# Performance work log

Hardware: AMD Instinct MI355X
Metric: run time of the kernel (lower is better)

Reference implementation:

```python
import jax, jax.numpy as jnp
import numpy as np

B, S, H = 512, 14, 128  # batch, encoder seq_len (hardcoded 14 in source), hidden
IN = 1                  # input_size must be 1 (see decoder permute trick)


def lstm_scan(seq, h0, c0, Wih, Whh, b):
    """seq: [T, B, in]. Returns (all_h [T,B,H], h_T, c_T). torch gate order i,f,g,o."""
    def step(carry, x_t):
        h, c = carry
        g = x_t @ Wih + h @ Whh + b              # [B, 4H]
        i, f, gg, o = jnp.split(g, 4, axis=-1)
        c = jax.nn.sigmoid(f) * c + jax.nn.sigmoid(i) * jnp.tanh(gg)
        h = jax.nn.sigmoid(o) * jnp.tanh(c)
        return (h, c), h
    (h, c), hs = jax.lax.scan(step, (h0, c0), seq)
    return hs, h, c


def setup_inputs() -> dict:
    key = jax.random.key(0)
    ks = jax.random.split(key, 12)
    s = 1.0 / np.sqrt(H)
    return {
        "inputs": jax.random.normal(ks[0], (B, S, IN), dtype=jnp.float32),
        "target_len": 8,
        "Wih_e": jax.random.normal(ks[1], (IN, 4 * H), dtype=jnp.float32) * s,
        "Whh_e": jax.random.normal(ks[2], (H, 4 * H), dtype=jnp.float32) * s,
        "b_e":   jax.random.normal(ks[3], (4 * H,), dtype=jnp.float32) * s,
        "Wih_d": jax.random.normal(ks[4], (IN, 4 * H), dtype=jnp.float32) * s,
        "Whh_d": jax.random.normal(ks[5], (H, 4 * H), dtype=jnp.float32) * s,
        "b_d":   jax.random.normal(ks[6], (4 * H,), dtype=jnp.float32) * s,
        "We": jax.random.normal(ks[7], (H, H), dtype=jnp.float32) * s,
        "Wd": jax.random.normal(ks[8], (H, H), dtype=jnp.float32) * s,
        "Wv": jax.random.normal(ks[9], (H, 1), dtype=jnp.float32) * s,
        "Wf": jax.random.normal(ks[10], (H, IN), dtype=jnp.float32) * s,
        "bf": jax.random.normal(ks[11], (IN,), dtype=jnp.float32) * s,
    }


def reference(inputs, target_len, Wih_e, Whh_e, b_e, Wih_d, Whh_d, b_d, We, Wd, Wv, Wf, bf):
    bs = inputs.shape[0]
    h0 = jnp.zeros((bs, H), inputs.dtype)
    c0 = jnp.zeros((bs, H), inputs.dtype)

    # Encoder: LSTM over the S=14 timesteps.
    hs, h_enc, c_enc = lstm_scan(inputs.transpose(1, 0, 2), h0, c0, Wih_e, Whh_e, b_e)
    enc_out = hs.transpose(1, 0, 2)  # [B, S, H]

    def dec_step(carry, _):
        x, h, c = carry  # x: [B, 1]
        # Bahdanau additive attention (recomputes enc projection each step, as in source).
        e = jnp.tanh(enc_out @ We + (h @ Wd)[:, None, :])   # [B, S, H]
        attn = jax.nn.softmax(e @ Wv, axis=1)               # [B, S, 1]
        context = jnp.sum(attn * enc_out, axis=1)           # [B, H]
        # new_input = cat(context, x) then permute -> sequence of H+1 scalars.
        seq = jnp.concatenate([context, x], axis=1).T[:, :, None]  # [H+1, B, 1]
        _, h, c = lstm_scan(seq, h, c, Wih_d, Whh_d, b_d)
        out = h @ Wf + bf  # output[:, -1, :] == final hidden -> fin_linear, [B, 1]
        return (out, h, c), (out, attn)

    (_, _, _), (outs, attns) = jax.lax.scan(
        dec_step, (inputs[:, -1, :], h_enc, c_enc), None, length=target_len)
    outputs = outs.transpose(1, 0, 2)      # [B, target_len, 1]
    total_attn = jnp.sum(attns, axis=0)    # [B, S, 1]
    return outputs, total_attn
```

## Files before the change

### kernel.cpp

```cpp
#include <hip/hip_runtime.h>

#define HDIM 128
#define SEQ  14
#define G4   512
#define TLEN 8
#define NTHR 512
#define HPITCH 160

typedef _Float16 half8 __attribute__((ext_vector_type(8)));
typedef float f32x4 __attribute__((ext_vector_type(4)));
typedef float f32x2 __attribute__((ext_vector_type(2)));

#define LOG2E  1.44269504f
#define LOG2E2 2.88539008f

__device__ __forceinline__ float frcp_(float x) { return __builtin_amdgcn_rcpf(x); }
#if defined(__has_builtin)
#if __has_builtin(__builtin_amdgcn_exp2f)
#define EXP2_(x) __builtin_amdgcn_exp2f(x)
#endif
#endif
#ifndef EXP2_
#define EXP2_(x) __expf((x) * 0.69314718f)
#endif
__device__ __forceinline__ float fsigP_(float y)  { return frcp_(1.0f + EXP2_(-y)); }
__device__ __forceinline__ float ftanhP_(float y) { return 1.0f - 2.0f * frcp_(EXP2_(y) + 1.0f); }
__device__ __forceinline__ float ftanh_(float x)  { return ftanhP_(x * LOG2E2); }

struct __align__(16) SMem {
    __align__(16) float zq[4];
    _Float16 h2[2][2][HPITCH];
    _Float16 ench[SEQ][2][HPITCH];
    _Float16 encWe[SEQ][2][HDIM];
    _Float16 hWdh[2][HDIM];
    __align__(16) float ctx2[HDIM + 1][2];
    __align__(16) float inp2[SEQ][2];
    float attnw[2][SEQ];
    float asum[2][SEQ];
    float score[2][SEQ];
    float wv[HDIM];
    float wf[HDIM];
};

__device__ __forceinline__ float lstm_core(
    const _Float16* __restrict__ srcBase,
    _Float16* __restrict__ dstw,
    f32x2 xv, f32x4 zeroq,
    const half8 (&whh)[4][4], const float (&wih)[4], const float (&bia)[4],
    float& c, int q, int l)
{
    const _Float16* sp = srcBase + ((l >> 2) & 1) * HPITCH + 8 * q;
    half8 a0 = *(const half8*)(sp);
    half8 a1 = *(const half8*)(sp + 32);
    half8 a2 = *(const half8*)(sp + 64);
    half8 a3 = *(const half8*)(sp + 96);
    f32x4 A[4];
    #pragma unroll
    for (int g = 0; g < 4; ++g) {
        A[g] = __builtin_amdgcn_mfma_f32_16x16x32_f16(a0, whh[g][0], zeroq, 0, 0, 0);
        A[g] = __builtin_amdgcn_mfma_f32_16x16x32_f16(a1, whh[g][1], A[g], 0, 0, 0);
        A[g] = __builtin_amdgcn_mfma_f32_16x16x32_f16(a2, whh[g][2], A[g], 0, 0, 0);
        A[g] = __builtin_amdgcn_mfma_f32_16x16x32_f16(a3, whh[g][3], A[g], 0, 0, 0);
    }
    float hn = 0.0f;
    if (q < 2) {
        float x = (q & 1) ? xv[1] : xv[0];
        float ig = fsigP_(fmaf(x, wih[0], bia[0]) + A[0][0]);
        float fg = fsigP_(fmaf(x, wih[1], bia[1]) + A[1][0]);
        float gg = ftanhP_(fmaf(x, wih[2], bia[2]) + A[2][0]);
        float og = fsigP_(fmaf(x, wih[3], bia[3]) + A[3][0]);
        c = fmaf(fg, c, ig * gg);
        hn = og * ftanhP_(c * LOG2E2);
        *dstw = (_Float16)hn;
    }
    return hn;
}

__global__ __launch_bounds__(NTHR, 2) void seq2seq_kernel(
    const float* __restrict__ inputs,
    const float* __restrict__ Wih_e, const float* __restrict__ Whh_e, const float* __restrict__ b_e,
    const float* __restrict__ Wih_d, const float* __restrict__ Whh_d, const float* __restrict__ b_d,
    const float* __restrict__ We, const float* __restrict__ Wd,
    const float* __restrict__ Wv, const float* __restrict__ Wf, const float* __restrict__ bfp,
    float* __restrict__ out, int B)
{
    const int tid  = threadIdx.x;
    const int b0   = blockIdx.x * 2;
    const int w    = tid >> 6;
    const int lane = tid & 63;
    const int q    = lane >> 4;
    const int l    = lane & 15;
    const int wrcol = 16 * w + l;
    __shared__ SMem S;

    const _Float16* s0 = &S.h2[0][0][0];
    const _Float16* s1 = &S.h2[1][0][0];
    _Float16* d0 = &S.h2[0][q & 1][wrcol];
    _Float16* d1 = &S.h2[1][q & 1][wrcol];

    const float gscale[4] = {LOG2E, LOG2E, LOG2E2, LOG2E};

    if (tid < 4) S.zq[tid] = 0.0f;
    if (tid < 2 * HDIM) {
        int e = tid >> 7, j = tid & 127;
        S.h2[0][e][j] = (_Float16)0.0f;
        S.h2[1][e][j] = (_Float16)0.0f;
    }
    if (tid < SEQ * 2) {
        int t = tid >> 1, m = tid & 1;
        S.inp2[t][m] = inputs[(b0 + m) * SEQ + t];
        S.asum[m][t] = 0.0f;
    }
    if (tid < HDIM) { S.wv[tid] = Wv[tid]; S.wf[tid] = Wf[tid]; }
    if (tid < 2) S.ctx2[HDIM][tid] = inputs[(b0 + tid) * SEQ + (SEQ - 1)];

    half8 whh[4][4];
    float wih[4], bia[4];
    #pragma unroll
    for (int g = 0; g < 4; ++g) {
        int n = g * HDIM + wrcol;
        float sc = gscale[g];
        wih[g] = Wih_e[n] * sc;
        bia[g] = b_e[n] * sc;
        #pragma unroll
        for (int kt = 0; kt < 4; ++kt) {
            half8 f;
            #pragma unroll
            for (int jj = 0; jj < 8; ++jj)
                f[jj] = (_Float16)(Whh_e[(32 * kt + 8 * q + jj) * G4 + n] * sc);
            whh[g][kt] = f;
        }
    }
    float c = 0.0f;
    __syncthreads();

    const f32x4 zeroq = *(const f32x4*)S.zq;

    f32x2 xv = *(const f32x2*)&S.inp2[0][0];
    for (int t = 0; t < SEQ; t += 2) {
        float hn = lstm_core(s0, d1, xv, zeroq, whh, wih, bia, c, q, l);
        if (q < 2) S.ench[t][q][wrcol] = (_Float16)hn;
        xv = *(const f32x2*)&S.inp2[t + 1][0];
        __syncthreads();
        hn = lstm_core(s1, d0, xv, zeroq, whh, wih, bia, c, q, l);
        if (q < 2) S.ench[t + 1][q][wrcol] = (_Float16)hn;
        if (t + 2 < SEQ) xv = *(const f32x2*)&S.inp2[t + 2][0];
        __syncthreads();
    }

    {
        half8 wef[4];
        #pragma unroll
        for (int kt = 0; kt < 4; ++kt) {
            half8 f;
            #pragma unroll
            for (int jj = 0; jj < 8; ++jj)
                f[jj] = (_Float16)We[(32 * kt + 8 * q + jj) * HDIM + wrcol];
            wef[kt] = f;
        }
        for (int t = 0; t < SEQ; ++t) {
            const _Float16* er = &S.ench[t][0][0] + ((l >> 2) & 1) * HPITCH + 8 * q;
            f32x4 dv = zeroq;
            #pragma unroll
            for (int kt = 0; kt < 4; ++kt) {
                half8 a = *(const half8*)(er + 32 * kt);
                dv = __builtin_amdgcn_mfma_f32_16x16x32_f16(a, wef[kt], dv, 0, 0, 0);
            }
            if (q < 2) S.encWe[t][q][wrcol] = (_Float16)dv[0];
        }
    }

    half8 wdf[4];
    #pragma unroll
    for (int g = 0; g < 4; ++g) {
        int n = g * HDIM + wrcol;
        float sc = gscale[g];
        wih[g] = Wih_d[n] * sc;
        bia[g] = b_d[n] * sc;
        #pragma unroll
        for (int kt = 0; kt < 4; ++kt) {
            half8 f;
            #pragma unroll
            for (int jj = 0; jj < 8; ++jj)
                f[jj] = (_Float16)(Whh_d[(32 * kt + 8 * q + jj) * G4 + n] * sc);
            whh[g][kt] = f;
        }
    }
    #pragma unroll
    for (int kt = 0; kt < 4; ++kt) {
        half8 f;
        #pragma unroll
        for (int jj = 0; jj < 8; ++jj)
            f[jj] = (_Float16)Wd[(32 * kt + 8 * q + jj) * HDIM + wrcol];
        wdf[kt] = f;
    }
    float bf0 = bfp[0];
    __syncthreads();

    #pragma unroll 1
    for (int dd = 0; dd < TLEN; ++dd) {
        const bool even = (dd & 1) == 0;
        const _Float16* sC = even ? s0 : s1;
        const _Float16* sO = even ? s1 : s0;
        _Float16* dC = even ? d0 : d1;
        _Float16* dO = even ? d1 : d0;

        {
            const _Float16* sp = sC + ((l >> 2) & 1) * HPITCH + 8 * q;
            half8 a0 = *(const half8*)(sp);
            half8 a1 = *(const half8*)(sp + 32);
            half8 a2 = *(const half8*)(sp + 64);
            half8 a3 = *(const half8*)(sp + 96);
            f32x4 dv = zeroq;
            dv = __builtin_amdgcn_mfma_f32_16x16x32_f16(a0, wdf[0], dv, 0, 0, 0);
            dv = __builtin_amdgcn_mfma_f32_16x16x32_f16(a1, wdf[1], dv, 0, 0, 0);
            dv = __builtin_amdgcn_mfma_f32_16x16x32_f16(a2, wdf[2], dv, 0, 0, 0);
            dv = __builtin_amdgcn_mfma_f32_16x16x32_f16(a3, wdf[3], dv, 0, 0, 0);
            if (q < 2) S.hWdh[q][wrcol] = (_Float16)dv[0];
        }
        __syncthreads();
        if (tid < 2 * SEQ * 16) {
            int p = tid >> 4, sub = tid & 15;
            int m = p & 1, t = p >> 1;
            float s = 0.0f;
            #pragma unroll
            for (int i = 0; i < 8; ++i) {
                int j = sub * 8 + i;
                s = fmaf(ftanh_((float)S.encWe[t][m][j] + (float)S.hWdh[m][j]), S.wv[j], s);
            }
            s += __shfl_down(s, 8, 16);
            s += __shfl_down(s, 4, 16);
            s += __shfl_down(s, 2, 16);
            s += __shfl_down(s, 1, 16);
            if (sub == 0) S.score[m][t] = s;
        }
        __syncthreads();
        if (tid < 2) {
            int m = tid;
            float sc[SEQ]; float mx = -1e30f;
            #pragma unroll
            for (int t = 0; t < SEQ; ++t) { sc[t] = S.score[m][t]; mx = fmaxf(mx, sc[t]); }
            float ssum = 0.0f;
            #pragma unroll
            for (int t = 0; t < SEQ; ++t) { float e = __expf(sc[t] - mx); sc[t] = e; ssum += e; }
            float inv = frcp_(ssum);
            #pragma unroll
            for (int t = 0; t < SEQ; ++t) {
                float a = sc[t] * inv;
                S.attnw[m][t] = a;
                S.asum[m][t] += a;
            }
        }
        __syncthreads();
        if (tid < 256) {
            int e = tid >> 7, j = tid & 127;
            float a = 0.0f;
            #pragma unroll
            for (int t = 0; t < SEQ; ++t)
                a = fmaf(S.attnw[e][t], (float)S.ench[t][e][j], a);
            S.ctx2[j][e] = a;
        }
        __syncthreads();

        const f32x2* xp = (const f32x2*)&S.ctx2[0][0];
        f32x2 xd = xp[0];
        #pragma unroll 1
        for (int s2 = 0; s2 < 64; ++s2) {
            (void)lstm_core(sC, dO, xd, zeroq, whh, wih, bia, c, q, l);
            xd = xp[2 * s2 + 1];
            __syncthreads();
            (void)lstm_core(sO, dC, xd, zeroq, whh, wih, bia, c, q, l);
            xd = xp[2 * s2 + 2];
            __syncthreads();
        }
        (void)lstm_core(sC, dO, xd, zeroq, whh, wih, bia, c, q, l);
        __syncthreads();
        const _Float16* hO = even ? &S.h2[1][0][0] : &S.h2[0][0][0];
        if (tid < 32) {
            int m = tid >> 4, part = tid & 15;
            half8 hv = *(const half8*)(hO + m * HPITCH + part * 8);
            float s = 0.0f;
            #pragma unroll
            for (int i = 0; i < 8; ++i) s = fmaf((float)hv[i], S.wf[part * 8 + i], s);
            s += __shfl_down(s, 8, 16);
            s += __shfl_down(s, 4, 16);
            s += __shfl_down(s, 2, 16);
            s += __shfl_down(s, 1, 16);
            if (part == 0) {
                float o = s + bf0;
                out[(b0 + m) * TLEN + dd] = o;
                S.ctx2[HDIM][m] = o;
            }
        }
        __syncthreads();
    }

    if (tid < 2 * SEQ) {
        int m = tid / SEQ, t = tid % SEQ;
        out[B * TLEN + (b0 + m) * SEQ + t] = S.asum[m][t];
    }
}

extern "C" void kernel_launch(void* const* d_in, const int* in_sizes, int n_in,
                              void* d_out, int out_size, void* d_ws, size_t ws_size,
                              hipStream_t stream) {
    const float* inputs = (const float*)d_in[0];
    const float* Wih_e = (const float*)d_in[2];
    const float* Whh_e = (const float*)d_in[3];
    const float* b_e   = (const float*)d_in[4];
    const float* Wih_d = (const float*)d_in[5];
    const float* Whh_d = (const float*)d_in[6];
    const float* b_d   = (const float*)d_in[7];
    const float* We    = (const float*)d_in[8];
    const float* Wd    = (const float*)d_in[9];
    const float* Wv    = (const float*)d_in[10];
    const float* Wf    = (const float*)d_in[11];
    const float* bfp   = (const float*)d_in[12];
    float* out = (float*)d_out;

    const int B = in_sizes[0] / SEQ;

    seq2seq_kernel<<<dim3(B / 2), dim3(NTHR), 0, stream>>>(
        inputs, Wih_e, Whh_e, b_e, Wih_d, Whh_d, b_d, We, Wd, Wv, Wf, bfp, out, B);
}
```

Before: 507.5 us.

## Halve block to 256 threads with two column tiles per wave

Shrinks each block from 8 waves to 4, so every wave owns two 16-column tiles per gate. Each wave now issues twice the MFMAs and two cell updates per timestep, and register weight storage doubles (whh becomes [4][2][4]). The aim is cheaper __syncthreads barriers across the 129-step sequential decoder recurrence, since fewer waves have to synchronise. In exchange the per-step critical path per wave gets longer, and higher register use lowers occupancy to one block per CU in the launch bounds.

New measurement: 623.8 us. +22.9%, slower.

```diff
diff --git a/kernel.cpp b/kernel.cpp
--- a/kernel.cpp
+++ b/kernel.cpp
@@ -4,7 +4,7 @@
 #define SEQ  14
 #define G4   512
 #define TLEN 8
-#define NTHR 512
+#define NTHR 256
 #define HPITCH 160
 
 typedef _Float16 half8 __attribute__((ext_vector_type(8)));
@@ -42,41 +42,57 @@
     float wf[HDIM];
 };
 
-__device__ __forceinline__ float lstm_core(
+__device__ __forceinline__ f32x2 lstm_core2(
     const _Float16* __restrict__ srcBase,
-    _Float16* __restrict__ dstw,
+    _Float16* __restrict__ dstA,
+    _Float16* __restrict__ dstB,
     f32x2 xv, f32x4 zeroq,
-    const half8 (&whh)[4][4], const float (&wih)[4], const float (&bia)[4],
-    float& c, int q, int l)
+    const half8 (&whh)[4][2][4], const float (&wih)[4][2], const float (&bia)[4][2],
+    float& cA, float& cB, int q, int l)
 {
     const _Float16* sp = srcBase + ((l >> 2) & 1) * HPITCH + 8 * q;
     half8 a0 = *(const half8*)(sp);
     half8 a1 = *(const half8*)(sp + 32);
     half8 a2 = *(const half8*)(sp + 64);
     half8 a3 = *(const half8*)(sp + 96);
-    f32x4 A[4];
+    f32x4 A[4][2];
     #pragma unroll
     for (int g = 0; g < 4; ++g) {
-        A[g] = __builtin_amdgcn_mfma_f32_16x16x32_f16(a0, whh[g][0], zeroq, 0, 0, 0);
-        A[g] = __builtin_amdgcn_mfma_f32_16x16x32_f16(a1, whh[g][1], A[g], 0, 0, 0);
-        A[g] = __builtin_amdgcn_mfma_f32_16x16x32_f16(a2, whh[g][2], A[g], 0, 0, 0);
-        A[g] = __builtin_amdgcn_mfma_f32_16x16x32_f16(a3, whh[g][3], A[g], 0, 0, 0);
-    }
-    float hn = 0.0f;
+        #pragma unroll
+        for (int tl = 0; tl < 2; ++tl) {
+            f32x4 acc = __builtin_amdgcn_mfma_f32_16x16x32_f16(a0, whh[g][tl][0], zeroq, 0, 0, 0);
+            acc = __builtin_amdgcn_mfma_f32_16x16x32_f16(a1, whh[g][tl][1], acc, 0, 0, 0);
+            acc = __builtin_amdgcn_mfma_f32_16x16x32_f16(a2, whh[g][tl][2], acc, 0, 0, 0);
+            acc = __builtin_amdgcn_mfma_f32_16x16x32_f16(a3, whh[g][tl][3], acc, 0, 0, 0);
+            A[g][tl] = acc;
+        }
+    }
+    f32x2 hn; hn[0] = 0.0f; hn[1] = 0.0f;
     if (q < 2) {
         float x = (q & 1) ? xv[1] : xv[0];
-        float ig = fsigP_(fmaf(x, wih[0], bia[0]) + A[0][0]);
-        float fg = fsigP_(fmaf(x, wih[1], bia[1]) + A[1][0]);
-        float gg = ftanhP_(fmaf(x, wih[2], bia[2]) + A[2][0]);
-        float og = fsigP_(fmaf(x, wih[3], bia[3]) + A[3][0]);
-        c = fmaf(fg, c, ig * gg);
-        hn = og * ftanhP_(c * LOG2E2);
-        *dstw = (_Float16)hn;
+        {
+            float ig = fsigP_(fmaf(x, wih[0][0], bia[0][0]) + A[0][0][0]);
+            float fg = fsigP_(fmaf(x, wih[1][0], bia[1][0]) + A[1][0][0]);
+            float gv = ftanhP_(fmaf(x, wih[2][0], bia[2][0]) + A[2][0][0]);
+            float og = fsigP_(fmaf(x, wih[3][0], bia[3][0]) + A[3][0][0]);
+            cA = fmaf(fg, cA, ig * gv);
+            hn[0] = og * ftanhP_(cA * LOG2E2);
+            *dstA = (_Float16)hn[0];
+        }
+        {
+            float ig = fsigP_(fmaf(x, wih[0][1], bia[0][1]) + A[0][1][0]);
+            float fg = fsigP_(fmaf(x, wih[1][1], bia[1][1]) + A[1][1][0]);
+            float gv = ftanhP_(fmaf(x, wih[2][1], bia[2][1]) + A[2][1][0]);
+            float og = fsigP_(fmaf(x, wih[3][1], bia[3][1]) + A[3][1][0]);
+            cB = fmaf(fg, cB, ig * gv);
+            hn[1] = og * ftanhP_(cB * LOG2E2);
+            *dstB = (_Float16)hn[1];
+        }
     }
     return hn;
 }
 
-__global__ __launch_bounds__(NTHR, 2) void seq2seq_kernel(
+__global__ __launch_bounds__(NTHR, 1) void seq2seq_kernel(
     const float* __restrict__ inputs,
     const float* __restrict__ Wih_e, const float* __restrict__ Whh_e, const float* __restrict__ b_e,
     const float* __restrict__ Wih_d, const float* __restrict__ Whh_d, const float* __restrict__ b_d,
@@ -90,13 +106,16 @@
     const int lane = tid & 63;
     const int q    = lane >> 4;
     const int l    = lane & 15;
-    const int wrcol = 16 * w + l;
+    const int colA = 32 * w + l;
+    const int colB = colA + 16;
     __shared__ SMem S;
 
     const _Float16* s0 = &S.h2[0][0][0];
     const _Float16* s1 = &S.h2[1][0][0];
-    _Float16* d0 = &S.h2[0][q & 1][wrcol];
-    _Float16* d1 = &S.h2[1][q & 1][wrcol];
+    _Float16* d0A = &S.h2[0][q & 1][colA];
+    _Float16* d0B = &S.h2[0][q & 1][colB];
+    _Float16* d1A = &S.h2[1][q & 1][colA];
+    _Float16* d1B = &S.h2[1][q & 1][colB];
 
     const float gscale[4] = {LOG2E, LOG2E, LOG2E2, LOG2E};
 
@@ -114,86 +133,107 @@
     if (tid < HDIM) { S.wv[tid] = Wv[tid]; S.wf[tid] = Wf[tid]; }
     if (tid < 2) S.ctx2[HDIM][tid] = inputs[(b0 + tid) * SEQ + (SEQ - 1)];
 
-    half8 whh[4][4];
-    float wih[4], bia[4];
+    half8 whh[4][2][4];
+    float wih[4][2], bia[4][2];
     #pragma unroll
     for (int g = 0; g < 4; ++g) {
-        int n = g * HDIM + wrcol;
         float sc = gscale[g];
-        wih[g] = Wih_e[n] * sc;
-        bia[g] = b_e[n] * sc;
+        #pragma unroll
+        for (int tl = 0; tl < 2; ++tl) {
+            int n = g * HDIM + colA + 16 * tl;
+            wih[g][tl] = Wih_e[n] * sc;
+            bia[g][tl] = b_e[n] * sc;
+            #pragma unroll
+            for (int kt = 0; kt < 4; ++kt) {
+                half8 f;
+                #pragma unroll
+                for (int jj = 0; jj < 8; ++jj)
+                    f[jj] = (_Float16)(Whh_e[(32 * kt + 8 * q + jj) * G4 + n] * sc);
+                whh[g][tl][kt] = f;
+            }
+        }
+    }
+    float cA = 0.0f, cB = 0.0f;
+    __syncthreads();
+
+    const f32x4 zeroq = *(const f32x4*)S.zq;
+
+    f32x2 xv = *(const f32x2*)&S.inp2[0][0];
+    for (int t = 0; t < SEQ; t += 2) {
+        f32x2 hn = lstm_core2(s0, d1A, d1B, xv, zeroq, whh, wih, bia, cA, cB, q, l);
+        if (q < 2) {
+            S.ench[t][q][colA] = (_Float16)hn[0];
+            S.ench[t][q][colB] = (_Float16)hn[1];
+        }
+        xv = *(const f32x2*)&S.inp2[t + 1][0];
+        __syncthreads();
+        hn = lstm_core2(s1, d0A, d0B, xv, zeroq, whh, wih, bia, cA, cB, q, l);
+        if (q < 2) {
+            S.ench[t + 1][q][colA] = (_Float16)hn[0];
+            S.ench[t + 1][q][colB] = (_Float16)hn[1];
+        }
+        if (t + 2 < SEQ) xv = *(const f32x2*)&S.inp2[t + 2][0];
+        __syncthreads();
+    }
+
+    {
+        half8 wef[2][4];
+        #pragma unroll
+        for (int tl = 0; tl < 2; ++tl)
+            #pragma unroll
+            for (int kt = 0; kt < 4; ++kt) {
+                half8 f;
+                #pragma unroll
+                for (int jj = 0; jj < 8; ++jj)
+                    f[jj] = (_Float16)We[(32 * kt + 8 * q + jj) * HDIM + colA + 16 * tl];
+                wef[tl][kt] = f;
+            }
+        for (int t = 0; t < SEQ; ++t) {
+            const _Float16* er = &S.ench[t][0][0] + ((l >> 2) & 1) * HPITCH + 8 * q;
+            half8 e0 = *(const half8*)(er);
+            half8 e1 = *(const half8*)(er + 32);
+            half8 e2 = *(const half8*)(er + 64);
+            half8 e3 = *(const half8*)(er + 96);
+            #pragma unroll
+            for (int tl = 0; tl < 2; ++tl) {
+                f32x4 dv = __builtin_amdgcn_mfma_f32_16x16x32_f16(e0, wef[tl][0], zeroq, 0, 0, 0);
+                dv = __builtin_amdgcn_mfma_f32_16x16x32_f16(e1, wef[tl][1], dv, 0, 0, 0);
+                dv = __builtin_amdgcn_mfma_f32_16x16x32_f16(e2, wef[tl][2], dv, 0, 0, 0);
+                dv = __builtin_amdgcn_mfma_f32_16x16x32_f16(e3, wef[tl][3], dv, 0, 0, 0);
+                if (q < 2) S.encWe[t][q][colA + 16 * tl] = (_Float16)dv[0];
+            }
+        }
+    }
+
+    half8 wdf[2][4];
+    #pragma unroll
+    for (int g = 0; g < 4; ++g) {
+        float sc = gscale[g];
+        #pragma unroll
+        for (int tl = 0; tl < 2; ++tl) {
+            int n = g * HDIM + colA + 16 * tl;
+            wih[g][tl] = Wih_d[n] * sc;
+            bia[g][tl] = b_d[n] * sc;
+            #pragma unroll
+            for (int kt = 0; kt < 4; ++kt) {
+                half8 f;
+                #pragma unroll
+                for (int jj = 0; jj < 8; ++jj)
+                    f[jj] = (_Float16)(Whh_d[(32 * kt + 8 * q + jj) * G4 + n] * sc);
+                whh[g][tl][kt] = f;
+            }
+        }
+    }
+    #pragma unroll
+    for (int tl = 0; tl < 2; ++tl)
         #pragma unroll
         for (int kt = 0; kt < 4; ++kt) {
             half8 f;
             #pragma unroll
             for (int jj = 0; jj < 8; ++jj)
-                f[jj] = (_Float16)(Whh_e[(32 * kt + 8 * q + jj) * G4 + n] * sc);
-            whh[g][kt] = f;
-        }
-    }
-    float c = 0.0f;
-    __syncthreads();
-
-    const f32x4 zeroq = *(const f32x4*)S.zq;
-
-    f32x2 xv = *(const f32x2*)&S.inp2[0][0];
-    for (int t = 0; t < SEQ; t += 2) {
-        float hn = lstm_core(s0, d1, xv, zeroq, whh, wih, bia, c, q, l);
-        if (q < 2) S.ench[t][q][wrcol] = (_Float16)hn;
-        xv = *(const f32x2*)&S.inp2[t + 1][0];
-        __syncthreads();
-        hn = lstm_core(s1, d0, xv, zeroq, whh, wih, bia, c, q, l);
-        if (q < 2) S.ench[t + 1][q][wrcol] = (_Float16)hn;
-        if (t + 2 < SEQ) xv = *(const f32x2*)&S.inp2[t + 2][0];
-        __syncthreads();
-    }
-
-    {
-        half8 wef[4];
-        #pragma unroll
-        for (int kt = 0; kt < 4; ++kt) {
-            half8 f;
-            #pragma unroll
-            for (int jj = 0; jj < 8; ++jj)
-                f[jj] = (_Float16)We[(32 * kt + 8 * q + jj) * HDIM + wrcol];
-            wef[kt] = f;
-        }
-        for (int t = 0; t < SEQ; ++t) {
-            const _Float16* er = &S.ench[t][0][0] + ((l >> 2) & 1) * HPITCH + 8 * q;
-            f32x4 dv = zeroq;
-            #pragma unroll
-            for (int kt = 0; kt < 4; ++kt) {
-                half8 a = *(const half8*)(er + 32 * kt);
-                dv = __builtin_amdgcn_mfma_f32_16x16x32_f16(a, wef[kt], dv, 0, 0, 0);
-            }
-            if (q < 2) S.encWe[t][q][wrcol] = (_Float16)dv[0];
-        }
-    }
-
-    half8 wdf[4];
-    #pragma unroll
-    for (int g = 0; g < 4; ++g) {
-        int n = g * HDIM + wrcol;
-        float sc = gscale[g];
-        wih[g] = Wih_d[n] * sc;
-        bia[g] = b_d[n] * sc;
-        #pragma unroll
-        for (int kt = 0; kt < 4; ++kt) {
-            half8 f;
-            #pragma unroll
-            for (int jj = 0; jj < 8; ++jj)
-                f[jj] = (_Float16)(Whh_d[(32 * kt + 8 * q + jj) * G4 + n] * sc);
-            whh[g][kt] = f;
-        }
-    }
-    #pragma unroll
-    for (int kt = 0; kt < 4; ++kt) {
-        half8 f;
-        #pragma unroll
-        for (int jj = 0; jj < 8; ++jj)
-            f[jj] = (_Float16)Wd[(32 * kt + 8 * q + jj) * HDIM + wrcol];
-        wdf[kt] = f;
-    }
+                f[jj] = (_Float16)Wd[(32 * kt + 8 * q + jj) * HDIM + colA + 16 * tl];
+            wdf[tl][kt] = f;
+        }
     float bf0 = bfp[0];
     __syncthreads();
 
@@ -202,8 +242,10 @@
         const bool even = (dd & 1) == 0;
         const _Float16* sC = even ? s0 : s1;
         const _Float16* sO = even ? s1 : s0;
-        _Float16* dC = even ? d0 : d1;
-        _Float16* dO = even ? d1 : d0;
+        _Float16* dCA = even ? d0A : d1A;
+        _Float16* dCB = even ? d0B : d1B;
+        _Float16* dOA = even ? d1A : d0A;
+        _Float16* dOB = even ? d1B : d0B;
 
         {
             const _Float16* sp = sC + ((l >> 2) & 1) * HPITCH + 8 * q;
@@ -211,27 +253,28 @@
             half8 a1 = *(const half8*)(sp + 32);
             half8 a2 = *(const half8*)(sp + 64);
             half8 a3 = *(const half8*)(sp + 96);
-            f32x4 dv = zeroq;
-            dv = __builtin_amdgcn_mfma_f32_16x16x32_f16(a0, wdf[0], dv, 0, 0, 0);
-            dv = __builtin_amdgcn_mfma_f32_16x16x32_f16(a1, wdf[1], dv, 0, 0, 0);
-            dv = __builtin_amdgcn_mfma_f32_16x16x32_f16(a2, wdf[2], dv, 0, 0, 0);
-            dv = __builtin_amdgcn_mfma_f32_16x16x32_f16(a3, wdf[3], dv, 0, 0, 0);
-            if (q < 2) S.hWdh[q][wrcol] = (_Float16)dv[0];
-        }
-        __syncthreads();
-        if (tid < 2 * SEQ * 16) {
-            int p = tid >> 4, sub = tid & 15;
+            #pragma unroll
+            for (int tl = 0; tl < 2; ++tl) {
+                f32x4 dv = __builtin_amdgcn_mfma_f32_16x16x32_f16(a0, wdf[tl][0], zeroq, 0, 0, 0);
+                dv = __builtin_amdgcn_mfma_f32_16x16x32_f16(a1, wdf[tl][1], dv, 0, 0, 0);
+                dv = __builtin_amdgcn_mfma_f32_16x16x32_f16(a2, wdf[tl][2], dv, 0, 0, 0);
+                dv = __builtin_amdgcn_mfma_f32_16x16x32_f16(a3, wdf[tl][3], dv, 0, 0, 0);
+                if (q < 2) S.hWdh[q][colA + 16 * tl] = (_Float16)dv[0];
+            }
+        }
+        __syncthreads();
+        if (tid < 2 * SEQ * 8) {
+            int p = tid >> 3, sub = tid & 7;
             int m = p & 1, t = p >> 1;
             float s = 0.0f;
             #pragma unroll
-            for (int i = 0; i < 8; ++i) {
-                int j = sub * 8 + i;
+            for (int i = 0; i < 16; ++i) {
+                int j = sub * 16 + i;
                 s = fmaf(ftanh_((float)S.encWe[t][m][j] + (float)S.hWdh[m][j]), S.wv[j], s);
             }
-            s += __shfl_down(s, 8, 16);
-            s += __shfl_down(s, 4, 16);
-            s += __shfl_down(s, 2, 16);
-            s += __shfl_down(s, 1, 16);
+            s += __shfl_down(s, 4, 8);
+            s += __shfl_down(s, 2, 8);
+            s += __shfl_down(s, 1, 8);
             if (sub == 0) S.score[m][t] = s;
         }
         __syncthreads();
@@ -252,7 +295,7 @@
             }
         }
         __syncthreads();
-        if (tid < 256) {
+        {
             int e = tid >> 7, j = tid & 127;
             float a = 0.0f;
             #pragma unroll
@@ -266,14 +309,14 @@
         f32x2 xd = xp[0];
         #pragma unroll 1
         for (int s2 = 0; s2 < 64; ++s2) {
-            (void)lstm_core(sC, dO, xd, zeroq, whh, wih, bia, c, q, l);
+            (void)lstm_core2(sC, dOA, dOB, xd, zeroq, whh, wih, bia, cA, cB, q, l);
             xd = xp[2 * s2 + 1];
             __syncthreads();
-            (void)lstm_core(sO, dC, xd, zeroq, whh, wih, bia, c, q, l);
+            (void)lstm_core2(sO, dCA, dCB, xd, zeroq, whh, wih, bia, cA, cB, q, l);
             xd = xp[2 * s2 + 2];
             __syncthreads();
         }
-        (void)lstm_core(sC, dO, xd, zeroq, whh, wih, bia, c, q, l);
+        (void)lstm_core2(sC, dOA, dOB, xd, zeroq, whh, wih, bia, cA, cB, q, l);
         __syncthreads();
         const _Float16* hO = even ? &S.h2[1][0][0] : &S.h2[0][0][0];
         if (tid < 32) {
```

## Process two batch pairs per block, interleaving their LSTM recurrences

Applied to the files above, without the earlier changes.

Each block now handles four batch rows as two independent pairs with separate shared-memory state, interleaving their LSTM steps and attention work between barriers. This amortizes barrier and latency costs over two independent dependency chains. It halves the grid to B/4 blocks, leaving many CUs idle, and raises register and LDS use per block.

Measured after the change: 808.2 us. 1.59x slower.

```diff
diff --git a/kernel.cpp b/kernel.cpp
--- a/kernel.cpp
+++ b/kernel.cpp
@@ -27,8 +27,7 @@
 __device__ __forceinline__ float ftanhP_(float y) { return 1.0f - 2.0f * frcp_(EXP2_(y) + 1.0f); }
 __device__ __forceinline__ float ftanh_(float x)  { return ftanhP_(x * LOG2E2); }
 
-struct __align__(16) SMem {
-    __align__(16) float zq[4];
+struct __align__(16) PairMem {
     _Float16 h2[2][2][HPITCH];
     _Float16 ench[SEQ][2][HPITCH];
     _Float16 encWe[SEQ][2][HDIM];
@@ -38,29 +37,41 @@
     float attnw[2][SEQ];
     float asum[2][SEQ];
     float score[2][SEQ];
+};
+
+struct __align__(16) SMem {
+    __align__(16) float zq[4];
+    PairMem P[2];
     float wv[HDIM];
     float wf[HDIM];
 };
 
-__device__ __forceinline__ float lstm_core(
-    const _Float16* __restrict__ srcBase,
+struct AFrag { half8 a0, a1, a2, a3; };
+
+__device__ __forceinline__ AFrag lstm_read(const _Float16* __restrict__ srcBase, int q, int l) {
+    const _Float16* sp = srcBase + ((l >> 2) & 1) * HPITCH + 8 * q;
+    AFrag f;
+    f.a0 = *(const half8*)(sp);
+    f.a1 = *(const half8*)(sp + 32);
+    f.a2 = *(const half8*)(sp + 64);
+    f.a3 = *(const half8*)(sp + 96);
+    return f;
+}
+
+__device__ __forceinline__ float lstm_compute(
+    const AFrag& f,
     _Float16* __restrict__ dstw,
     f32x2 xv, f32x4 zeroq,
     const half8 (&whh)[4][4], const float (&wih)[4], const float (&bia)[4],
-    float& c, int q, int l)
+    float& c, int q)
 {
-    const _Float16* sp = srcBase + ((l >> 2) & 1) * HPITCH + 8 * q;
-    half8 a0 = *(const half8*)(sp);
-    half8 a1 = *(const half8*)(sp + 32);
-    half8 a2 = *(const half8*)(sp + 64);
-    half8 a3 = *(const half8*)(sp + 96);
     f32x4 A[4];
     #pragma unroll
     for (int g = 0; g < 4; ++g) {
-        A[g] = __builtin_amdgcn_mfma_f32_16x16x32_f16(a0, whh[g][0], zeroq, 0, 0, 0);
-        A[g] = __builtin_amdgcn_mfma_f32_16x16x32_f16(a1, whh[g][1], A[g], 0, 0, 0);
-        A[g] = __builtin_amdgcn_mfma_f32_16x16x32_f16(a2, whh[g][2], A[g], 0, 0, 0);
-        A[g] = __builtin_amdgcn_mfma_f32_16x16x32_f16(a3, whh[g][3], A[g], 0, 0, 0);
+        A[g] = __builtin_amdgcn_mfma_f32_16x16x32_f16(f.a0, whh[g][0], zeroq, 0, 0, 0);
+        A[g] = __builtin_amdgcn_mfma_f32_16x16x32_f16(f.a1, whh[g][1], A[g], 0, 0, 0);
+        A[g] = __builtin_amdgcn_mfma_f32_16x16x32_f16(f.a2, whh[g][2], A[g], 0, 0, 0);
+        A[g] = __builtin_amdgcn_mfma_f32_16x16x32_f16(f.a3, whh[g][3], A[g], 0, 0, 0);
     }
     float hn = 0.0f;
     if (q < 2) {
@@ -85,7 +96,7 @@
     float* __restrict__ out, int B)
 {
     const int tid  = threadIdx.x;
-    const int b0   = blockIdx.x * 2;
+    const int b0   = blockIdx.x * 4;
     const int w    = tid >> 6;
     const int lane = tid & 63;
     const int q    = lane >> 4;
@@ -93,26 +104,31 @@
     const int wrcol = 16 * w + l;
     __shared__ SMem S;
 
-    const _Float16* s0 = &S.h2[0][0][0];
-    const _Float16* s1 = &S.h2[1][0][0];
-    _Float16* d0 = &S.h2[0][q & 1][wrcol];
-    _Float16* d1 = &S.h2[1][q & 1][wrcol];
+    const _Float16* s0A = &S.P[0].h2[0][0][0];
+    const _Float16* s1A = &S.P[0].h2[1][0][0];
+    const _Float16* s0B = &S.P[1].h2[0][0][0];
+    const _Float16* s1B = &S.P[1].h2[1][0][0];
+    _Float16* d0A = &S.P[0].h2[0][q & 1][wrcol];
+    _Float16* d1A = &S.P[0].h2[1][q & 1][wrcol];
+    _Float16* d0B = &S.P[1].h2[0][q & 1][wrcol];
+    _Float16* d1B = &S.P[1].h2[1][q & 1][wrcol];
 
     const float gscale[4] = {LOG2E, LOG2E, LOG2E2, LOG2E};
 
     if (tid < 4) S.zq[tid] = 0.0f;
-    if (tid < 2 * HDIM) {
-        int e = tid >> 7, j = tid & 127;
-        S.h2[0][e][j] = (_Float16)0.0f;
-        S.h2[1][e][j] = (_Float16)0.0f;
-    }
-    if (tid < SEQ * 2) {
-        int t = tid >> 1, m = tid & 1;
-        S.inp2[t][m] = inputs[(b0 + m) * SEQ + t];
-        S.asum[m][t] = 0.0f;
+    for (int idx = tid; idx < 2 * 2 * 2 * HDIM; idx += NTHR) {
+        int p = idx >> 9, r = idx & 511;
+        int buf = r >> 8, e = (r >> 7) & 1, j = r & 127;
+        S.P[p].h2[buf][e][j] = (_Float16)0.0f;
+    }
+    if (tid < SEQ * 4) {
+        int t = tid >> 2, mm = tid & 3;
+        int p = mm >> 1, m = mm & 1;
+        S.P[p].inp2[t][m] = inputs[(b0 + mm) * SEQ + t];
+        S.P[p].asum[m][t] = 0.0f;
     }
     if (tid < HDIM) { S.wv[tid] = Wv[tid]; S.wf[tid] = Wf[tid]; }
-    if (tid < 2) S.ctx2[HDIM][tid] = inputs[(b0 + tid) * SEQ + (SEQ - 1)];
+    if (tid < 4) S.P[tid >> 1].ctx2[HDIM][tid & 1] = inputs[(b0 + tid) * SEQ + (SEQ - 1)];
 
     half8 whh[4][4];
     float wih[4], bia[4];
@@ -131,20 +147,37 @@
             whh[g][kt] = f;
         }
     }
-    float c = 0.0f;
+    float cA = 0.0f, cB = 0.0f;
     __syncthreads();
 
     const f32x4 zeroq = *(const f32x4*)S.zq;
 
-    f32x2 xv = *(const f32x2*)&S.inp2[0][0];
+    f32x2 xvA = *(const f32x2*)&S.P[0].inp2[0][0];
+    f32x2 xvB = *(const f32x2*)&S.P[1].inp2[0][0];
     for (int t = 0; t < SEQ; t += 2) {
-        float hn = lstm_core(s0, d1, xv, zeroq, whh, wih, bia, c, q, l);
-        if (q < 2) S.ench[t][q][wrcol] = (_Float16)hn;
-        xv = *(const f32x2*)&S.inp2[t + 1][0];
-        __syncthreads();
-        hn = lstm_core(s1, d0, xv, zeroq, whh, wih, bia, c, q, l);
-        if (q < 2) S.ench[t + 1][q][wrcol] = (_Float16)hn;
-        if (t + 2 < SEQ) xv = *(const f32x2*)&S.inp2[t + 2][0];
+        AFrag fA = lstm_read(s0A, q, l);
+        AFrag fB = lstm_read(s0B, q, l);
+        float hnA = lstm_compute(fA, d1A, xvA, zeroq, whh, wih, bia, cA, q);
+        float hnB = lstm_compute(fB, d1B, xvB, zeroq, whh, wih, bia, cB, q);
+        if (q < 2) {
+            S.P[0].ench[t][q][wrcol] = (_Float16)hnA;
+            S.P[1].ench[t][q][wrcol] = (_Float16)hnB;
+        }
+        xvA = *(const f32x2*)&S.P[0].inp2[t + 1][0];
+        xvB = *(const f32x2*)&S.P[1].inp2[t + 1][0];
+        __syncthreads();
+        fA = lstm_read(s1A, q, l);
+        fB = lstm_read(s1B, q, l);
+        hnA = lstm_compute(fA, d0A, xvA, zeroq, whh, wih, bia, cA, q);
+        hnB = lstm_compute(fB, d0B, xvB, zeroq, whh, wih, bia, cB, q);
+        if (q < 2) {
+            S.P[0].ench[t + 1][q][wrcol] = (_Float16)hnA;
+            S.P[1].ench[t + 1][q][wrcol] = (_Float16)hnB;
+        }
+        if (t + 2 < SEQ) {
+            xvA = *(const f32x2*)&S.P[0].inp2[t + 2][0];
+            xvB = *(const f32x2*)&S.P[1].inp2[t + 2][0];
+        }
         __syncthreads();
     }
 
@@ -159,14 +192,19 @@
             wef[kt] = f;
         }
         for (int t = 0; t < SEQ; ++t) {
-            const _Float16* er = &S.ench[t][0][0] + ((l >> 2) & 1) * HPITCH + 8 * q;
-            f32x4 dv = zeroq;
-            #pragma unroll
-            for (int kt = 0; kt < 4; ++kt) {
-                half8 a = *(const half8*)(er + 32 * kt);
-                dv = __builtin_amdgcn_mfma_f32_16x16x32_f16(a, wef[kt], dv, 0, 0, 0);
-            }
-            if (q < 2) S.encWe[t][q][wrcol] = (_Float16)dv[0];
+            #pragma unroll
+            for (int p = 0; p < 2; ++p) {
+                const _Float16* er = &S.P[p].ench[t][0][0] + ((l >> 2) & 1) * HPITCH + 8 * q;
+                half8 e0 = *(const half8*)(er);
+                half8 e1 = *(const half8*)(er + 32);
+                half8 e2 = *(const half8*)(er + 64);
+                half8 e3 = *(const half8*)(er + 96);
+                f32x4 dv = __builtin_amdgcn_mfma_f32_16x16x32_f16(e0, wef[0], zeroq, 0, 0, 0);
+                dv = __builtin_amdgcn_mfma_f32_16x16x32_f16(e1, wef[1], dv, 0, 0, 0);
+                dv = __builtin_amdgcn_mfma_f32_16x16x32_f16(e2, wef[2], dv, 0, 0, 0);
+                dv = __builtin_amdgcn_mfma_f32_16x16x32_f16(e3, wef[3], dv, 0, 0, 0);
+                if (q < 2) S.P[p].encWe[t][q][wrcol] = (_Float16)dv[0];
+            }
         }
     }
 
@@ -200,46 +238,53 @@
     #pragma unroll 1
     for (int dd = 0; dd < TLEN; ++dd) {
         const bool even = (dd & 1) == 0;
-        const _Float16* sC = even ? s0 : s1;
-        const _Float16* sO = even ? s1 : s0;
-        _Float16* dC = even ? d0 : d1;
-        _Float16* dO = even ? d1 : d0;
+        const _Float16* sCA = even ? s0A : s1A;
+        const _Float16* sOA = even ? s1A : s0A;
+        const _Float16* sCB = even ? s0B : s1B;
+        const _Float16* sOB = even ? s1B : s0B;
+        _Float16* dCA = even ? d0A : d1A;
+        _Float16* dOA = even ? d1A : d0A;
+        _Float16* dCB = even ? d0B : d1B;
+        _Float16* dOB = even ? d1B : d0B;
 
         {
-            const _Float16* sp = sC + ((l >> 2) & 1) * HPITCH + 8 * q;
-            half8 a0 = *(const half8*)(sp);
-            half8 a1 = *(const half8*)(sp + 32);
-            half8 a2 = *(const half8*)(sp + 64);
-            half8 a3 = *(const half8*)(sp + 96);
-            f32x4 dv = zeroq;
-            dv = __builtin_amdgcn_mfma_f32_16x16x32_f16(a0, wdf[0], dv, 0, 0, 0);
-            dv = __builtin_amdgcn_mfma_f32_16x16x32_f16(a1, wdf[1], dv, 0, 0, 0);
-            dv = __builtin_amdgcn_mfma_f32_16x16x32_f16(a2, wdf[2], dv, 0, 0, 0);
-            dv = __builtin_amdgcn_mfma_f32_16x16x32_f16(a3, wdf[3], dv, 0, 0, 0);
-            if (q < 2) S.hWdh[q][wrcol] = (_Float16)dv[0];
-        }
-        __syncthreads();
-        if (tid < 2 * SEQ * 16) {
-            int p = tid >> 4, sub = tid & 15;
-            int m = p & 1, t = p >> 1;
+            AFrag fA = lstm_read(sCA, q, l);
+            AFrag fB = lstm_read(sCB, q, l);
+            f32x4 dvA = __builtin_amdgcn_mfma_f32_16x16x32_f16(fA.a0, wdf[0], zeroq, 0, 0, 0);
+            dvA = __builtin_amdgcn_mfma_f32_16x16x32_f16(fA.a1, wdf[1], dvA, 0, 0, 0);
+            dvA = __builtin_amdgcn_mfma_f32_16x16x32_f16(fA.a2, wdf[2], dvA, 0, 0, 0);
+            dvA = __builtin_amdgcn_mfma_f32_16x16x32_f16(fA.a3, wdf[3], dvA, 0, 0, 0);
+            f32x4 dvB = __builtin_amdgcn_mfma_f32_16x16x32_f16(fB.a0, wdf[0], zeroq, 0, 0, 0);
+            dvB = __builtin_amdgcn_mfma_f32_16x16x32_f16(fB.a1, wdf[1], dvB, 0, 0, 0);
+            dvB = __builtin_amdgcn_mfma_f32_16x16x32_f16(fB.a2, wdf[2], dvB, 0, 0, 0);
+            dvB = __builtin_amdgcn_mfma_f32_16x16x32_f16(fB.a3, wdf[3], dvB, 0, 0, 0);
+            if (q < 2) {
+                S.P[0].hWdh[q][wrcol] = (_Float16)dvA[0];
+                S.P[1].hWdh[q][wrcol] = (_Float16)dvB[0];
+            }
+        }
+        __syncthreads();
+        if (tid < 4 * SEQ * 8) {
+            int p8 = tid >> 3, sub = tid & 7;
+            int mm = p8 & 3, t = p8 >> 2;
+            int p = mm >> 1, m = mm & 1;
             float s = 0.0f;
             #pragma unroll
-            for (int i = 0; i < 8; ++i) {
-                int j = sub * 8 + i;
-                s = fmaf(ftanh_((float)S.encWe[t][m][j] + (float)S.hWdh[m][j]), S.wv[j], s);
-            }
-            s += __shfl_down(s, 8, 16);
-            s += __shfl_down(s, 4, 16);
-            s += __shfl_down(s, 2, 16);
-            s += __shfl_down(s, 1, 16);
-            if (sub == 0) S.score[m][t] = s;
-        }
-        __syncthreads();
-        if (tid < 2) {
-            int m = tid;
+            for (int i = 0; i < 16; ++i) {
+                int j = sub * 16 + i;
+                s = fmaf(ftanh_((float)S.P[p].encWe[t][m][j] + (float)S.P[p].hWdh[m][j]), S.wv[j], s);
+            }
+            s += __shfl_down(s, 4, 8);
+            s += __shfl_down(s, 2, 8);
+            s += __shfl_down(s, 1, 8);
+            if (sub == 0) S.P[p].score[m][t] = s;
+        }
+        __syncthreads();
+        if (tid < 4) {
+            int p = tid >> 1, m = tid & 1;
             float sc[SEQ]; float mx = -1e30f;
             #pragma unroll
-            for (int t = 0; t < SEQ; ++t) { sc[t] = S.score[m][t]; mx = fmaxf(mx, sc[t]); }
+            for (int t = 0; t < SEQ; ++t) { sc[t] = S.P[p].score[m][t]; mx = fmaxf(mx, sc[t]); }
             float ssum = 0.0f;
             #pragma unroll
             for (int t = 0; t < SEQ; ++t) { float e = __expf(sc[t] - mx); sc[t] = e; ssum += e; }
@@ -247,37 +292,54 @@
             #pragma unroll
             for (int t = 0; t < SEQ; ++t) {
                 float a = sc[t] * inv;
-                S.attnw[m][t] = a;
-                S.asum[m][t] += a;
-            }
-        }
-        __syncthreads();
-        if (tid < 256) {
-            int e = tid >> 7, j = tid & 127;
+                S.P[p].attnw[m][t] = a;
+                S.P[p].asum[m][t] += a;
+            }
+        }
+        __syncthreads();
+        {
+            int e4 = tid >> 7, j = tid & 127;
+            int p = e4 >> 1, e = e4 & 1;
             float a = 0.0f;
             #pragma unroll
             for (int t = 0; t < SEQ; ++t)
-                a = fmaf(S.attnw[e][t], (float)S.ench[t][e][j], a);
-            S.ctx2[j][e] = a;
-        }
-        __syncthreads();
-
-        const f32x2* xp = (const f32x2*)&S.ctx2[0][0];
-        f32x2 xd = xp[0];
+                a = fmaf(S.P[p].attnw[e][t], (float)S.P[p].ench[t][e][j], a);
+            S.P[p].ctx2[j][e] = a;
+        }
+        __syncthreads();
+
+        const f32x2* xpA = (const f32x2*)&S.P[0].ctx2[0][0];
+        const f32x2* xpB = (const f32x2*)&S.P[1].ctx2[0][0];
+        f32x2 xdA = xpA[0];
+        f32x2 xdB = xpB[0];
         #pragma unroll 1
         for (int s2 = 0; s2 < 64; ++s2) {
-            (void)lstm_core(sC, dO, xd, zeroq, whh, wih, bia, c, q, l);
-            xd = xp[2 * s2 + 1];
+            AFrag fA = lstm_read(sCA, q, l);
+            AFrag fB = lstm_read(sCB, q, l);
+            (void)lstm_compute(fA, dOA, xdA, zeroq, whh, wih, bia, cA, q);
+            (void)lstm_compute(fB, dOB, xdB, zeroq, whh, wih, bia, cB, q);
+            xdA = xpA[2 * s2 + 1];
+            xdB = xpB[2 * s2 + 1];
             __syncthreads();
-            (void)lstm_core(sO, dC, xd, zeroq, whh, wih, bia, c, q, l);
-            xd = xp[2 * s2 + 2];
+            fA = lstm_read(sOA, q, l);
+            fB = lstm_read(sOB, q, l);
+            (void)lstm_compute(fA, dCA, xdA, zeroq, whh, wih, bia, cA, q);
+            (void)lstm_compute(fB, dCB, xdB, zeroq, whh, wih, bia, cB, q);
+            xdA = xpA[2 * s2 + 2];
+            xdB = xpB[2 * s2 + 2];
             __syncthreads();
         }
-        (void)lstm_core(sC, dO, xd, zeroq, whh, wih, bia, c, q, l);
-        __syncthreads();
-        const _Float16* hO = even ? &S.h2[1][0][0] : &S.h2[0][0][0];
-        if (tid < 32) {
-            int m = tid >> 4, part = tid & 15;
+        {
+            AFrag fA = lstm_read(sCA, q, l);
+            AFrag fB = lstm_read(sCB, q, l);
+            (void)lstm_compute(fA, dOA, xdA, zeroq, whh, wih, bia, cA, q);
+            (void)lstm_compute(fB, dOB, xdB, zeroq, whh, wih, bia, cB, q);
+        }
+        __syncthreads();
+        if (tid < 64) {
+            int m4 = tid >> 4, part = tid & 15;
+            int p = m4 >> 1, m = m4 & 1;
+            const _Float16* hO = even ? &S.P[p].h2[1][0][0] : &S.P[p].h2[0][0][0];
             half8 hv = *(const half8*)(hO + m * HPITCH + part * 8);
             float s = 0.0f;
             #pragma unroll
@@ -288,16 +350,16 @@
             s += __shfl_down(s, 1, 16);
             if (part == 0) {
                 float o = s + bf0;
-                out[(b0 + m) * TLEN + dd] = o;
-                S.ctx2[HDIM][m] = o;
-            }
-        }
-        __syncthreads();
-    }
-
-    if (tid < 2 * SEQ) {
-        int m = tid / SEQ, t = tid % SEQ;
-        out[B * TLEN + (b0 + m) * SEQ + t] = S.asum[m][t];
+                out[(b0 + m4) * TLEN + dd] = o;
+                S.P[p].ctx2[HDIM][m] = o;
+            }
+        }
+        __syncthreads();
+    }
+
+    if (tid < 4 * SEQ) {
+        int m4 = tid / SEQ, t = tid % SEQ;
+        out[B * TLEN + (b0 + m4) * SEQ + t] = S.P[m4 >> 1].asum[m4 & 1][t];
     }
 }
 
@@ -320,6 +382,6 @@
 
     const int B = in_sizes[0] / SEQ;
 
-    seq2seq_kernel<<<dim3(B / 2), dim3(NTHR), 0, stream>>>(
+    seq2seq_kernel<<<dim3(B / 4), dim3(NTHR), 0, stream>>>(
         inputs, Wih_e, Whh_e, b_e, Wih_d, Whh_d, b_d, We, Wd, Wv, Wf, bfp, out, B);
 }
```

## Pack two batch pairs per 1024-thread block with separate shared state

Applied to the files above, without the earlier changes.

Each block now runs 1024 threads, with two independent 512-thread halves each handling its own pair of batch rows and its own shared-memory region. The grid is halved and the launch bounds drop to one block per CU-slot. The intent is to share weight broadcasts and fill more waves per block. The cost is that __syncthreads now couples both halves, and register pressure changes under the new launch bounds; occupancy may be similar to running two 512-thread blocks before.

New measurement: 833.5 us. 64.2% more time.

```diff
diff --git a/kernel.cpp b/kernel.cpp
--- a/kernel.cpp
+++ b/kernel.cpp
@@ -4,7 +4,7 @@
 #define SEQ  14
 #define G4   512
 #define TLEN 8
-#define NTHR 512
+#define NTHR 1024
 #define HPITCH 160
 
 typedef _Float16 half8 __attribute__((ext_vector_type(8)));
@@ -27,8 +27,7 @@
 __device__ __forceinline__ float ftanhP_(float y) { return 1.0f - 2.0f * frcp_(EXP2_(y) + 1.0f); }
 __device__ __forceinline__ float ftanh_(float x)  { return ftanhP_(x * LOG2E2); }
 
-struct __align__(16) SMem {
-    __align__(16) float zq[4];
+struct __align__(16) PairMem {
     _Float16 h2[2][2][HPITCH];
     _Float16 ench[SEQ][2][HPITCH];
     _Float16 encWe[SEQ][2][HDIM];
@@ -38,6 +37,11 @@
     float attnw[2][SEQ];
     float asum[2][SEQ];
     float score[2][SEQ];
+};
+
+struct __align__(16) SMem {
+    __align__(16) float zq[4];
+    PairMem P[2];
     float wv[HDIM];
     float wf[HDIM];
 };
@@ -76,7 +80,7 @@
     return hn;
 }
 
-__global__ __launch_bounds__(NTHR, 2) void seq2seq_kernel(
+__global__ __launch_bounds__(NTHR, 1) void seq2seq_kernel(
     const float* __restrict__ inputs,
     const float* __restrict__ Wih_e, const float* __restrict__ Whh_e, const float* __restrict__ b_e,
     const float* __restrict__ Wih_d, const float* __restrict__ Whh_d, const float* __restrict__ b_d,
@@ -85,34 +89,36 @@
     float* __restrict__ out, int B)
 {
     const int tid  = threadIdx.x;
-    const int b0   = blockIdx.x * 2;
-    const int w    = tid >> 6;
+    const int p    = tid >> 9;
+    const int t5   = tid & 511;
+    const int b0   = blockIdx.x * 4 + 2 * p;
+    const int w    = t5 >> 6;
     const int lane = tid & 63;
     const int q    = lane >> 4;
     const int l    = lane & 15;
     const int wrcol = 16 * w + l;
     __shared__ SMem S;
-
-    const _Float16* s0 = &S.h2[0][0][0];
-    const _Float16* s1 = &S.h2[1][0][0];
-    _Float16* d0 = &S.h2[0][q & 1][wrcol];
-    _Float16* d1 = &S.h2[1][q & 1][wrcol];
+    PairMem* __restrict__ PP = &S.P[p];
+
+    const _Float16* s0 = &PP->h2[0][0][0];
+    const _Float16* s1 = &PP->h2[1][0][0];
+    _Float16* d0 = &PP->h2[0][q & 1][wrcol];
+    _Float16* d1 = &PP->h2[1][q & 1][wrcol];
 
     const float gscale[4] = {LOG2E, LOG2E, LOG2E2, LOG2E};
 
     if (tid < 4) S.zq[tid] = 0.0f;
-    if (tid < 2 * HDIM) {
-        int e = tid >> 7, j = tid & 127;
-        S.h2[0][e][j] = (_Float16)0.0f;
-        S.h2[1][e][j] = (_Float16)0.0f;
-    }
-    if (tid < SEQ * 2) {
-        int t = tid >> 1, m = tid & 1;
-        S.inp2[t][m] = inputs[(b0 + m) * SEQ + t];
-        S.asum[m][t] = 0.0f;
+    if (t5 < 512) {
+        int buf = t5 >> 8, e = (t5 >> 7) & 1, j = t5 & 127;
+        PP->h2[buf][e][j] = (_Float16)0.0f;
+    }
+    if (t5 < SEQ * 2) {
+        int t = t5 >> 1, m = t5 & 1;
+        PP->inp2[t][m] = inputs[(b0 + m) * SEQ + t];
+        PP->asum[m][t] = 0.0f;
     }
     if (tid < HDIM) { S.wv[tid] = Wv[tid]; S.wf[tid] = Wf[tid]; }
-    if (tid < 2) S.ctx2[HDIM][tid] = inputs[(b0 + tid) * SEQ + (SEQ - 1)];
+    if (t5 < 2) PP->ctx2[HDIM][t5] = inputs[(b0 + t5) * SEQ + (SEQ - 1)];
 
     half8 whh[4][4];
     float wih[4], bia[4];
@@ -136,15 +142,15 @@
 
     const f32x4 zeroq = *(const f32x4*)S.zq;
 
-    f32x2 xv = *(const f32x2*)&S.inp2[0][0];
+    f32x2 xv = *(const f32x2*)&PP->inp2[0][0];
     for (int t = 0; t < SEQ; t += 2) {
         float hn = lstm_core(s0, d1, xv, zeroq, whh, wih, bia, c, q, l);
-        if (q < 2) S.ench[t][q][wrcol] = (_Float16)hn;
-        xv = *(const f32x2*)&S.inp2[t + 1][0];
+        if (q < 2) PP->ench[t][q][wrcol] = (_Float16)hn;
+        xv = *(const f32x2*)&PP->inp2[t + 1][0];
         __syncthreads();
         hn = lstm_core(s1, d0, xv, zeroq, whh, wih, bia, c, q, l);
-        if (q < 2) S.ench[t + 1][q][wrcol] = (_Float16)hn;
-        if (t + 2 < SEQ) xv = *(const f32x2*)&S.inp2[t + 2][0];
+        if (q < 2) PP->ench[t + 1][q][wrcol] = (_Float16)hn;
+        if (t + 2 < SEQ) xv = *(const f32x2*)&PP->inp2[t + 2][0];
         __syncthreads();
     }
 
@@ -159,14 +165,14 @@
             wef[kt] = f;
         }
         for (int t = 0; t < SEQ; ++t) {
-            const _Float16* er = &S.ench[t][0][0] + ((l >> 2) & 1) * HPITCH + 8 * q;
+            const _Float16* er = &PP->ench[t][0][0] + ((l >> 2) & 1) * HPITCH + 8 * q;
             f32x4 dv = zeroq;
             #pragma unroll
             for (int kt = 0; kt < 4; ++kt) {
                 half8 a = *(const half8*)(er + 32 * kt);
                 dv = __builtin_amdgcn_mfma_f32_16x16x32_f16(a, wef[kt], dv, 0, 0, 0);
             }
-            if (q < 2) S.encWe[t][q][wrcol] = (_Float16)dv[0];
+            if (q < 2) PP->encWe[t][q][wrcol] = (_Float16)dv[0];
         }
     }
 
@@ -216,30 +222,30 @@
             dv = __builtin_amdgcn_mfma_f32_16x16x32_f16(a1, wdf[1], dv, 0, 0, 0);
             dv = __builtin_amdgcn_mfma_f32_16x16x32_f16(a2, wdf[2], dv, 0, 0, 0);
             dv = __builtin_amdgcn_mfma_f32_16x16x32_f16(a3, wdf[3], dv, 0, 0, 0);
-            if (q < 2) S.hWdh[q][wrcol] = (_Float16)dv[0];
-        }
-        __syncthreads();
-        if (tid < 2 * SEQ * 16) {
-            int p = tid >> 4, sub = tid & 15;
-            int m = p & 1, t = p >> 1;
+            if (q < 2) PP->hWdh[q][wrcol] = (_Float16)dv[0];
+        }
+        __syncthreads();
+        if (t5 < 2 * SEQ * 16) {
+            int pr = t5 >> 4, sub = t5 & 15;
+            int m = pr & 1, t = pr >> 1;
             float s = 0.0f;
             #pragma unroll
             for (int i = 0; i < 8; ++i) {
                 int j = sub * 8 + i;
-                s = fmaf(ftanh_((float)S.encWe[t][m][j] + (float)S.hWdh[m][j]), S.wv[j], s);
+                s = fmaf(ftanh_((float)PP->encWe[t][m][j] + (float)PP->hWdh[m][j]), S.wv[j], s);
             }
             s += __shfl_down(s, 8, 16);
             s += __shfl_down(s, 4, 16);
             s += __shfl_down(s, 2, 16);
             s += __shfl_down(s, 1, 16);
-            if (sub == 0) S.score[m][t] = s;
-        }
-        __syncthreads();
-        if (tid < 2) {
-            int m = tid;
+            if (sub == 0) PP->score[m][t] = s;
+        }
+        __syncthreads();
+        if (t5 < 2) {
+            int m = t5;
             float sc[SEQ]; float mx = -1e30f;
             #pragma unroll
-            for (int t = 0; t < SEQ; ++t) { sc[t] = S.score[m][t]; mx = fmaxf(mx, sc[t]); }
+            for (int t = 0; t < SEQ; ++t) { sc[t] = PP->score[m][t]; mx = fmaxf(mx, sc[t]); }
             float ssum = 0.0f;
             #pragma unroll
             for (int t = 0; t < SEQ; ++t) { float e = __expf(sc[t] - mx); sc[t] = e; ssum += e; }
@@ -247,22 +253,22 @@
             #pragma unroll
             for (int t = 0; t < SEQ; ++t) {
                 float a = sc[t] * inv;
-                S.attnw[m][t] = a;
-                S.asum[m][t] += a;
+                PP->attnw[m][t] = a;
+                PP->asum[m][t] += a;
             }
         }
         __syncthreads();
-        if (tid < 256) {
-            int e = tid >> 7, j = tid & 127;
+        if (t5 < 256) {
+            int e = t5 >> 7, j = t5 & 127;
             float a = 0.0f;
             #pragma unroll
             for (int t = 0; t < SEQ; ++t)
-                a = fmaf(S.attnw[e][t], (float)S.ench[t][e][j], a);
-            S.ctx2[j][e] = a;
-        }
-        __syncthreads();
-
-        const f32x2* xp = (const f32x2*)&S.ctx2[0][0];
+                a = fmaf(PP->attnw[e][t], (float)PP->ench[t][e][j], a);
+            PP->ctx2[j][e] = a;
+        }
+        __syncthreads();
+
+        const f32x2* xp = (const f32x2*)&PP->ctx2[0][0];
         f32x2 xd = xp[0];
         #pragma unroll 1
         for (int s2 = 0; s2 < 64; ++s2) {
@@ -275,9 +281,9 @@
         }
         (void)lstm_core(sC, dO, xd, zeroq, whh, wih, bia, c, q, l);
         __syncthreads();
-        const _Float16* hO = even ? &S.h2[1][0][0] : &S.h2[0][0][0];
-        if (tid < 32) {
-            int m = tid >> 4, part = tid & 15;
+        const _Float16* hO = even ? &PP->h2[1][0][0] : &PP->h2[0][0][0];
+        if (t5 < 32) {
+            int m = t5 >> 4, part = t5 & 15;
             half8 hv = *(const half8*)(hO + m * HPITCH + part * 8);
             float s = 0.0f;
             #pragma unroll
@@ -289,15 +295,15 @@
             if (part == 0) {
                 float o = s + bf0;
                 out[(b0 + m) * TLEN + dd] = o;
-                S.ctx2[HDIM][m] = o;
+                PP->ctx2[HDIM][m] = o;
             }
         }
         __syncthreads();
     }
 
-    if (tid < 2 * SEQ) {
-        int m = tid / SEQ, t = tid % SEQ;
-        out[B * TLEN + (b0 + m) * SEQ + t] = S.asum[m][t];
+    if (t5 < 2 * SEQ) {
+        int m = t5 / SEQ, t = t5 % SEQ;
+        out[B * TLEN + (b0 + m) * SEQ + t] = PP->asum[m][t];
     }
 }
 
@@ -320,6 +326,6 @@
 
     const int B = in_sizes[0] / SEQ;
 
-    seq2seq_kernel<<<dim3(B / 2), dim3(NTHR), 0, stream>>>(
+    seq2seq_kernel<<<dim3(B / 4), dim3(NTHR), 0, stream>>>(
         inputs, Wih_e, Whh_e, b_e, Wih_d, Whh_d, b_d, We, Wd, Wv, Wf, bfp, out, B);
 }
```
